# Kernel tuning notes

Measured on AMD Instinct MI355X. Metric: run time of the kernel, lower is better.

The kernel has to match this reference:

```python
import jax, jax.numpy as jnp
import numpy as np

N, IN_DIM, OUT_DIM = 8192, 1024, 256
AVG_DEG = 32


def _w(key, shape, scale=0.05):
    return jax.random.normal(key, shape, dtype=jnp.float32) * scale


def setup_inputs() -> dict:
    key = jax.random.key(0)
    ks = jax.random.split(key, 20)
    x = jax.random.normal(ks[0], (N, IN_DIM), dtype=jnp.float32)
    # binary adjacency with average degree ~AVG_DEG (adj_matrix_to_edge_index
    # only keeps indices, so edge weights are effectively 1)
    A_pos = (jax.random.uniform(ks[1], (N, N)) < (AVG_DEG / N)).astype(jnp.float32)
    d = {"x": x, "A_pos": A_pos}
    # Linear layers (stored as [in, out]; y = x @ W + b)
    d["W1"], d["b1"] = _w(ks[2], (IN_DIM, 256)), jnp.zeros((256,), jnp.float32)
    d["W2"], d["b2"] = _w(ks[3], (256, 62)), jnp.zeros((62,), jnp.float32)
    d["W3"], d["b3"] = _w(ks[4], (62, OUT_DIM)), jnp.zeros((OUT_DIM,), jnp.float32)
    # GCNConv weights/biases
    d["G1"], d["gb1"] = _w(ks[5], (256, 256)), jnp.zeros((256,), jnp.float32)
    d["G2"], d["gb2"] = _w(ks[6], (62, 62)), jnp.zeros((62,), jnp.float32)
    for i, k in zip(range(3, 7), ks[7:11]):
        d[f"G{i}"], d[f"gb{i}"] = _w(k, (OUT_DIM, OUT_DIM)), jnp.zeros((OUT_DIM,), jnp.float32)
    return d


def _gcn_forward(x, A_pos, W1, b1, W2, b2, W3, b3,
                 G1, gb1, G2, gb2, G3, gb3, G4, gb4, G5, gb5, G6, gb6):
    n = x.shape[0]
    # GCN symmetric normalization with self loops: D^{-1/2}(A+I)D^{-1/2}
    A_hat = A_pos + jnp.eye(n, dtype=x.dtype)
    deg = A_hat.sum(axis=1)
    dinv = jnp.where(deg > 0, deg ** -0.5, 0.0)
    A_norm = dinv[:, None] * A_hat * dinv[None, :]

    def gcn(h, W, b):
        return A_norm @ (h @ W) + b

    x1_lin = x @ W1 + b1
    x1 = x1_lin + jax.nn.relu(gcn(x1_lin, G1, gb1))
    x2_lin = x1 @ W2 + b2
    x2 = x2_lin + jax.nn.relu(gcn(x2_lin, G2, gb2))
    x3_lin = x2 @ W3 + b3
    w = 0.5  # self.weight before *= 0.5
    x3 = x3_lin + w * jax.nn.relu(gcn(x3_lin, G3, gb3))
    x4 = x3 + w * jax.nn.relu(gcn(x4_in := x3, G4, gb4))
    w = w * 0.5  # self.weight *= 0.5
    x5 = x4 + w * jax.nn.relu(gcn(x4, G5, gb5))
    x6 = x5 + w * gcn(x5, G6, gb6)
    return x6


def reference(x, A_pos, W1, b1, W2, b2, W3, b3,
              G1, gb1, G2, gb2, G3, gb3, G4, gb4, G5, gb5, G6, gb6):
    return _gcn_forward(x, A_pos, W1, b1, W2, b2, W3, b3,
                        G1, gb1, G2, gb2, G3, gb3, G4, gb4, G5, gb5, G6, gb6)
```

## Files before the change

kernel.cpp:

```cpp
#include <hip/hip_runtime.h>
#include <hip/hip_bf16.h>
#include <stddef.h>
#include <stdint.h>

#define NROWS 8192
#define MAXD 128

typedef __attribute__((ext_vector_type(8))) short bf16x8;
typedef __attribute__((ext_vector_type(4))) float f32x4;
typedef __attribute__((ext_vector_type(4))) unsigned short u16x4;

static __device__ __forceinline__ unsigned short f2bf(float f) {
    unsigned int u = __float_as_uint(f);
    unsigned int r = (u + 0x7FFFu + ((u >> 16) & 1u)) >> 16;
    return (unsigned short)r;
}
static __device__ __forceinline__ float bf2f(unsigned short h) {
    return __uint_as_float(((unsigned int)h) << 16);
}

__global__ __launch_bounds__(256) void build_adj(
    const float* __restrict__ A, int* __restrict__ ell,
    int* __restrict__ cnt, float* __restrict__ dinv)
{
    int row = blockIdx.x;
    const float4* arow = (const float4*)(A + (size_t)row * NROWS);
    __shared__ int scnt;
    if (threadIdx.x == 0) scnt = 0;
    __syncthreads();
    int* erow = ell + (size_t)row * MAXD;
    for (int q = threadIdx.x; q < NROWS / 4; q += 256) {
        float4 v = arow[q];
        int j = q * 4;
        if (v.x != 0.f) { int s = atomicAdd(&scnt, 1); if (s < MAXD) erow[s] = j; }
        if (v.y != 0.f) { int s = atomicAdd(&scnt, 1); if (s < MAXD) erow[s] = j + 1; }
        if (v.z != 0.f) { int s = atomicAdd(&scnt, 1); if (s < MAXD) erow[s] = j + 2; }
        if (v.w != 0.f) { int s = atomicAdd(&scnt, 1); if (s < MAXD) erow[s] = j + 3; }
    }
    __syncthreads();
    if (threadIdx.x == 0) {
        int c = scnt; if (c > MAXD) c = MAXD;
        cnt[row] = c;
        dinv[row] = rsqrtf((float)scnt + 1.0f);
    }
}

__global__ __launch_bounds__(256) void tconv(
    const float* __restrict__ W, unsigned short* __restrict__ ht,
    unsigned short* __restrict__ lt, int K, int N, int Kpad, int Npad)
{
    int idx = blockIdx.x * 256 + threadIdx.x;
    if (idx >= Npad * Kpad) return;
    int n = idx / Kpad, k = idx % Kpad;
    float v = (k < K && n < N) ? W[(size_t)k * N + n] : 0.f;
    unsigned short hv = f2bf(v);
    ht[idx] = hv;
    lt[idx] = f2bf(v - bf2f(hv));
}

__global__ void pad64(const float* __restrict__ src, float* __restrict__ dst, int n)
{
    int i = threadIdx.x;
    dst[i] = (i < n) ? src[i] : 0.f;
}

__global__ __launch_bounds__(256) void gemm_mfma(
    const float* __restrict__ A,
    const unsigned short* __restrict__ Bth, const unsigned short* __restrict__ Btl,
    const float* __restrict__ bias,
    float* __restrict__ C, int K, int N)
{
    __shared__ __attribute__((aligned(16))) char smem[49152];
    const int tid = threadIdx.x;
    const int lane = tid & 63;
    const int w = tid >> 6;
    const int bm0 = blockIdx.x * 128;
    const int bn0 = blockIdx.y * 64;
    const int m_off = (w & 1) * 64;
    const int n_off = (w >> 1) * 32;

    f32x4 acc[4][2];
#pragma unroll
    for (int i = 0; i < 4; i++)
#pragma unroll
        for (int j = 0; j < 2; j++) acc[i][j] = (f32x4){0.f, 0.f, 0.f, 0.f};

    for (int k0 = 0; k0 < K; k0 += 64) {
#pragma unroll
        for (int i = 0; i < 8; ++i) {
            int q = tid + i * 256;
            int row = q >> 4;
            int kq = (q & 15) * 4;
            f32x4 v = *(const f32x4*)(A + (size_t)(bm0 + row) * K + k0 + kq);
            u16x4 hv, lv;
#pragma unroll
            for (int j = 0; j < 4; ++j) {
                unsigned short hh = f2bf(v[j]);
                hv[j] = hh;
                lv[j] = f2bf(v[j] - bf2f(hh));
            }
            int logb = kq * 2;
            int swz = (row << 7) + (logb ^ ((row & 7) << 4));
            *(u16x4*)(smem + swz) = hv;
            *(u16x4*)(smem + 16384 + swz) = lv;
        }
#pragma unroll
        for (int i = 0; i < 4; ++i) {
            int c = tid + i * 256;
            int half = c >> 9;
            int cc = c & 511;
            int row = cc >> 3;
            int logb = (cc & 7) * 16;
            const unsigned short* s =
                (half ? Btl : Bth) + (size_t)(bn0 + row) * K + k0 + (logb >> 1);
            bf16x8 v = *(const bf16x8*)s;
            int swz = (row << 7) + (logb ^ ((row & 7) << 4));
            *(bf16x8*)(smem + 32768 + (half << 13) + swz) = v;
        }
        __syncthreads();

#pragma unroll
        for (int kk = 0; kk < 64; kk += 32) {
            bf16x8 ah[4], al[4], bh[2], bl[2];
            int kb = (kk + ((lane >> 4) * 8)) * 2;
#pragma unroll
            for (int mi = 0; mi < 4; mi++) {
                int row = m_off + mi * 16 + (lane & 15);
                int off = (row << 7) + (kb ^ ((row & 7) << 4));
                ah[mi] = *(const bf16x8*)(smem + off);
                al[mi] = *(const bf16x8*)(smem + 16384 + off);
            }
#pragma unroll
            for (int ni = 0; ni < 2; ni++) {
                int row = n_off + ni * 16 + (lane & 15);
                int off = (row << 7) + (kb ^ ((row & 7) << 4));
                bh[ni] = *(const bf16x8*)(smem + 32768 + off);
                bl[ni] = *(const bf16x8*)(smem + 40960 + off);
            }
#pragma unroll
            for (int mi = 0; mi < 4; mi++)
#pragma unroll
                for (int ni = 0; ni < 2; ni++) {
                    acc[mi][ni] = __builtin_amdgcn_mfma_f32_16x16x32_bf16(ah[mi], bh[ni], acc[mi][ni], 0, 0, 0);
                    acc[mi][ni] = __builtin_amdgcn_mfma_f32_16x16x32_bf16(ah[mi], bl[ni], acc[mi][ni], 0, 0, 0);
                    acc[mi][ni] = __builtin_amdgcn_mfma_f32_16x16x32_bf16(al[mi], bh[ni], acc[mi][ni], 0, 0, 0);
                }
        }
        __syncthreads();
    }

#pragma unroll
    for (int mi = 0; mi < 4; mi++)
#pragma unroll
        for (int ni = 0; ni < 2; ni++) {
            int col = bn0 + n_off + ni * 16 + (lane & 15);
            float bv = bias ? bias[col] : 0.f;
            int rbase = bm0 + m_off + mi * 16 + ((lane >> 4) * 4);
#pragma unroll
            for (int r = 0; r < 4; r++)
                C[(size_t)(rbase + r) * N + col] = acc[mi][ni][r] + bv;
        }
}

__global__ __launch_bounds__(64) void spmm_vec4(
    const float* __restrict__ T, const int* __restrict__ ell,
    const int* __restrict__ cnt, const float* __restrict__ dinv,
    const float* __restrict__ base, const float* __restrict__ gb,
    float* __restrict__ out, float wscale, int do_relu)
{
    __shared__ int nb[MAXD];
    __shared__ float dv[MAXD];
    int row = blockIdx.x;
    int t = threadIdx.x;
    int c = cnt[row];
    for (int e = t; e < c; e += 64) {
        int j = ell[(size_t)row * MAXD + e];
        nb[e] = j;
        dv[e] = dinv[j];
    }
    __syncthreads();
    float di = dinv[row];
    f32x4 r = *(const f32x4*)(T + (size_t)row * 256 + t * 4) * di;
    f32x4 s1 = {0.f,0.f,0.f,0.f}, s2 = {0.f,0.f,0.f,0.f}, s3 = {0.f,0.f,0.f,0.f};
    int e = 0;
    for (; e + 4 <= c; e += 4) {
        r  += dv[e]     * *(const f32x4*)(T + (size_t)nb[e]     * 256 + t * 4);
        s1 += dv[e + 1] * *(const f32x4*)(T + (size_t)nb[e + 1] * 256 + t * 4);
        s2 += dv[e + 2] * *(const f32x4*)(T + (size_t)nb[e + 2] * 256 + t * 4);
        s3 += dv[e + 3] * *(const f32x4*)(T + (size_t)nb[e + 3] * 256 + t * 4);
    }
    for (; e < c; ++e)
        r += dv[e] * *(const f32x4*)(T + (size_t)nb[e] * 256 + t * 4);
    r = (r + s1) + (s2 + s3);
    f32x4 g = *(const f32x4*)(gb + t * 4);
    f32x4 b4 = *(const f32x4*)(base + (size_t)row * 256 + t * 4);
    f32x4 o4;
#pragma unroll
    for (int j = 0; j < 4; ++j) {
        float v = fmaf(di, r[j], g[j]);
        if (do_relu) v = fmaxf(v, 0.f);
        o4[j] = fmaf(wscale, v, b4[j]);
    }
    *(f32x4*)(out + (size_t)row * 256 + t * 4) = o4;
}

__global__ __launch_bounds__(64) void spmm64(
    const float* __restrict__ T, const int* __restrict__ ell,
    const int* __restrict__ cnt, const float* __restrict__ dinv,
    const float* __restrict__ base, const float* __restrict__ gb,
    float* __restrict__ out)
{
    __shared__ int nb[MAXD];
    __shared__ float dv[MAXD];
    int row = blockIdx.x;
    int f = threadIdx.x;
    int c = cnt[row];
    for (int e = f; e < c; e += 64) {
        int j = ell[(size_t)row * MAXD + e];
        nb[e] = j;
        dv[e] = dinv[j];
    }
    __syncthreads();
    float di = dinv[row];
    float r = di * T[(size_t)row * 64 + f];
    float p1 = 0.f, p2 = 0.f, p3 = 0.f;
    int e = 0;
    for (; e + 4 <= c; e += 4) {
        r  = fmaf(dv[e],     T[(size_t)nb[e]     * 64 + f], r);
        p1 = fmaf(dv[e + 1], T[(size_t)nb[e + 1] * 64 + f], p1);
        p2 = fmaf(dv[e + 2], T[(size_t)nb[e + 2] * 64 + f], p2);
        p3 = fmaf(dv[e + 3], T[(size_t)nb[e + 3] * 64 + f], p3);
    }
    for (; e < c; ++e) r = fmaf(dv[e], T[(size_t)nb[e] * 64 + f], r);
    r = (r + p1) + (p2 + p3);
    float v = fmaf(di, r, gb[f]);
    v = fmaxf(v, 0.f);
    out[(size_t)row * 64 + f] = v + base[(size_t)row * 64 + f];
}

static inline void mfma(const float* A, const unsigned short* Bth,
                        const unsigned short* Btl, const float* bias,
                        float* C, int K, int N, hipStream_t s)
{
    dim3 grid(NROWS / 128, N / 64);
    gemm_mfma<<<grid, 256, 0, s>>>(A, Bth, Btl, bias, C, K, N);
}

extern "C" void kernel_launch(void* const* d_in, const int* in_sizes, int n_in,
                              void* d_out, int out_size, void* d_ws, size_t ws_size,
                              hipStream_t stream)
{
    const float* x    = (const float*)d_in[0];
    const float* Apos = (const float*)d_in[1];
    const float* W1 = (const float*)d_in[2];  const float* b1  = (const float*)d_in[3];
    const float* W2 = (const float*)d_in[4];  const float* b2  = (const float*)d_in[5];
    const float* W3 = (const float*)d_in[6];  const float* b3  = (const float*)d_in[7];
    const float* G1 = (const float*)d_in[8];  const float* gb1 = (const float*)d_in[9];
    const float* G2 = (const float*)d_in[10]; const float* gb2 = (const float*)d_in[11];
    const float* G3 = (const float*)d_in[12]; const float* gb3 = (const float*)d_in[13];
    const float* G4 = (const float*)d_in[14]; const float* gb4 = (const float*)d_in[15];
    const float* G5 = (const float*)d_in[16]; const float* gb5 = (const float*)d_in[17];
    const float* G6 = (const float*)d_in[18]; const float* gb6 = (const float*)d_in[19];

    char* ws = (char*)d_ws;
    size_t off = 0;
    auto alloc = [&](size_t bytes) -> void* {
        void* p = ws + off;
        off = (off + bytes + 255) & ~(size_t)255;
        return p;
    };
    int*   ell  = (int*)  alloc((size_t)NROWS * MAXD * 4);
    int*   cnt  = (int*)  alloc((size_t)NROWS * 4);
    float* dinv = (float*)alloc((size_t)NROWS * 4);
    unsigned short* W1th = (unsigned short*)alloc(256 * 1024 * 2);
    unsigned short* W1tl = (unsigned short*)alloc(256 * 1024 * 2);
    unsigned short* W2th = (unsigned short*)alloc(64 * 256 * 2);
    unsigned short* W2tl = (unsigned short*)alloc(64 * 256 * 2);
    unsigned short* W3th = (unsigned short*)alloc(256 * 64 * 2);
    unsigned short* W3tl = (unsigned short*)alloc(256 * 64 * 2);
    unsigned short* G1th = (unsigned short*)alloc(256 * 256 * 2);
    unsigned short* G1tl = (unsigned short*)alloc(256 * 256 * 2);
    unsigned short* G2th = (unsigned short*)alloc(64 * 64 * 2);
    unsigned short* G2tl = (unsigned short*)alloc(64 * 64 * 2);
    unsigned short* G3th = (unsigned short*)alloc(256 * 256 * 2);
    unsigned short* G3tl = (unsigned short*)alloc(256 * 256 * 2);
    unsigned short* G4th = (unsigned short*)alloc(256 * 256 * 2);
    unsigned short* G4tl = (unsigned short*)alloc(256 * 256 * 2);
    unsigned short* G5th = (unsigned short*)alloc(256 * 256 * 2);
    unsigned short* G5tl = (unsigned short*)alloc(256 * 256 * 2);
    unsigned short* G6th = (unsigned short*)alloc(256 * 256 * 2);
    unsigned short* G6tl = (unsigned short*)alloc(256 * 256 * 2);
    float* b2p  = (float*)alloc(64 * 4);
    float* gb2p = (float*)alloc(64 * 4);
    float* lin  = (float*)alloc((size_t)NROWS * 256 * 4);
    float* T    = (float*)alloc((size_t)NROWS * 256 * 4);
    float* hA   = (float*)alloc((size_t)NROWS * 256 * 4);
    float* hB   = (float*)alloc((size_t)NROWS * 256 * 4);
    float* x2lin = lin;
    float* T62   = T;
    float* x2    = hB;
    float* outp = (float*)d_out;

    build_adj<<<NROWS, 256, 0, stream>>>(Apos, ell, cnt, dinv);

    tconv<<<(256 * 1024 + 255) / 256, 256, 0, stream>>>(W1, W1th, W1tl, 1024, 256, 1024, 256);
    tconv<<<(64 * 256 + 255) / 256, 256, 0, stream>>>(W2, W2th, W2tl, 256, 62, 256, 64);
    tconv<<<(256 * 64 + 255) / 256, 256, 0, stream>>>(W3, W3th, W3tl, 62, 256, 64, 256);
    tconv<<<(256 * 256 + 255) / 256, 256, 0, stream>>>(G1, G1th, G1tl, 256, 256, 256, 256);
    tconv<<<(64 * 64 + 255) / 256, 256, 0, stream>>>(G2, G2th, G2tl, 62, 62, 64, 64);
    tconv<<<(256 * 256 + 255) / 256, 256, 0, stream>>>(G3, G3th, G3tl, 256, 256, 256, 256);
    tconv<<<(256 * 256 + 255) / 256, 256, 0, stream>>>(G4, G4th, G4tl, 256, 256, 256, 256);
    tconv<<<(256 * 256 + 255) / 256, 256, 0, stream>>>(G5, G5th, G5tl, 256, 256, 256, 256);
    tconv<<<(256 * 256 + 255) / 256, 256, 0, stream>>>(G6, G6th, G6tl, 256, 256, 256, 256);
    pad64<<<1, 64, 0, stream>>>(b2, b2p, 62);
    pad64<<<1, 64, 0, stream>>>(gb2, gb2p, 62);

    mfma(x, W1th, W1tl, b1, lin, 1024, 256, stream);
    mfma(lin, G1th, G1tl, nullptr, T, 256, 256, stream);
    spmm_vec4<<<NROWS, 64, 0, stream>>>(T, ell, cnt, dinv, lin, gb1, hA, 1.0f, 1);
    mfma(hA, W2th, W2tl, b2p, x2lin, 256, 64, stream);
    mfma(x2lin, G2th, G2tl, nullptr, T62, 64, 64, stream);
    spmm64<<<NROWS, 64, 0, stream>>>(T62, ell, cnt, dinv, x2lin, gb2p, x2);
    mfma(x2, W3th, W3tl, b3, lin, 64, 256, stream);
    mfma(lin, G3th, G3tl, nullptr, T, 256, 256, stream);
    spmm_vec4<<<NROWS, 64, 0, stream>>>(T, ell, cnt, dinv, lin, gb3, hB, 0.5f, 1);
    mfma(hB, G4th, G4tl, nullptr, T, 256, 256, stream);
    spmm_vec4<<<NROWS, 64, 0, stream>>>(T, ell, cnt, dinv, hB, gb4, hA, 0.5f, 1);
    mfma(hA, G5th, G5tl, nullptr, T, 256, 256, stream);
    spmm_vec4<<<NROWS, 64, 0, stream>>>(T, ell, cnt, dinv, hA, gb5, hB, 0.25f, 1);
    mfma(hB, G6th, G6tl, nullptr, T, 256, 256, stream);
    spmm_vec4<<<NROWS, 64, 0, stream>>>(T, ell, cnt, dinv, hB, gb6, outp, 0.25f, 0);
}
```

Before: 812.7 us.

## Store GCN transform outputs as bf16 and gather bf16 in SpMM; batch weight conversions

The GEMM epilogue can now write its output as bf16. The sparse aggregation kernels gather neighbour rows from this bf16 buffer instead of fp32, which halves the bytes moved in the irregular neighbour gathers. The five 256x256 GCN weight conversions and the two bias pads are each merged into a single launch to cut launch count. In exchange, the intermediate h@W values lose precision to bf16 before aggregation, which adds numerical error.

New measurement: 747.3 us. 1.09x faster.

```diff
diff --git a/kernel.cpp b/kernel.cpp
--- a/kernel.cpp
+++ b/kernel.cpp
@@ -17,6 +17,14 @@
 }
 static __device__ __forceinline__ float bf2f(unsigned short h) {
     return __uint_as_float(((unsigned int)h) << 16);
+}
+static __device__ __forceinline__ f32x4 unpack4(uint2 u) {
+    f32x4 f;
+    f[0] = __uint_as_float(u.x << 16);
+    f[1] = __uint_as_float(u.x & 0xFFFF0000u);
+    f[2] = __uint_as_float(u.y << 16);
+    f[3] = __uint_as_float(u.y & 0xFFFF0000u);
+    return f;
 }
 
 __global__ __launch_bounds__(256) void build_adj(
@@ -58,17 +66,45 @@
     lt[idx] = f2bf(v - bf2f(hv));
 }
 
-__global__ void pad64(const float* __restrict__ src, float* __restrict__ dst, int n)
+__global__ __launch_bounds__(256) void tconvG5(
+    const float* __restrict__ g1, const float* __restrict__ g3,
+    const float* __restrict__ g4, const float* __restrict__ g5,
+    const float* __restrict__ g6,
+    unsigned short* __restrict__ h1, unsigned short* __restrict__ l1,
+    unsigned short* __restrict__ h3, unsigned short* __restrict__ l3,
+    unsigned short* __restrict__ h4, unsigned short* __restrict__ l4,
+    unsigned short* __restrict__ h5, unsigned short* __restrict__ l5,
+    unsigned short* __restrict__ h6, unsigned short* __restrict__ l6)
+{
+    const float* s; unsigned short* h; unsigned short* l;
+    switch (blockIdx.y) {
+        case 0:  s = g1; h = h1; l = l1; break;
+        case 1:  s = g3; h = h3; l = l3; break;
+        case 2:  s = g4; h = h4; l = l4; break;
+        case 3:  s = g5; h = h5; l = l5; break;
+        default: s = g6; h = h6; l = l6; break;
+    }
+    int idx = blockIdx.x * 256 + threadIdx.x;
+    int n = idx >> 8, k = idx & 255;
+    float v = s[(size_t)k * 256 + n];
+    unsigned short hv = f2bf(v);
+    h[idx] = hv;
+    l[idx] = f2bf(v - bf2f(hv));
+}
+
+__global__ void pad2(const float* __restrict__ b2, const float* __restrict__ gb2,
+                     float* __restrict__ b2p, float* __restrict__ gb2p)
 {
     int i = threadIdx.x;
-    dst[i] = (i < n) ? src[i] : 0.f;
+    if (i < 64) b2p[i] = (i < 62) ? b2[i] : 0.f;
+    else { int j = i - 64; gb2p[j] = (j < 62) ? gb2[j] : 0.f; }
 }
 
 __global__ __launch_bounds__(256) void gemm_mfma(
     const float* __restrict__ A,
     const unsigned short* __restrict__ Bth, const unsigned short* __restrict__ Btl,
     const float* __restrict__ bias,
-    float* __restrict__ C, int K, int N)
+    float* __restrict__ C, unsigned short* __restrict__ Cb, int K, int N)
 {
     __shared__ __attribute__((aligned(16))) char smem[49152];
     const int tid = threadIdx.x;
@@ -157,13 +193,17 @@
             float bv = bias ? bias[col] : 0.f;
             int rbase = bm0 + m_off + mi * 16 + ((lane >> 4) * 4);
 #pragma unroll
-            for (int r = 0; r < 4; r++)
-                C[(size_t)(rbase + r) * N + col] = acc[mi][ni][r] + bv;
+            for (int r = 0; r < 4; r++) {
+                float v = acc[mi][ni][r] + bv;
+                size_t idx = (size_t)(rbase + r) * N + col;
+                if (C)  C[idx]  = v;
+                if (Cb) Cb[idx] = f2bf(v);
+            }
         }
 }
 
-__global__ __launch_bounds__(64) void spmm_vec4(
-    const float* __restrict__ T, const int* __restrict__ ell,
+__global__ __launch_bounds__(64) void spmm_bf(
+    const unsigned short* __restrict__ Tb, const int* __restrict__ ell,
     const int* __restrict__ cnt, const float* __restrict__ dinv,
     const float* __restrict__ base, const float* __restrict__ gb,
     float* __restrict__ out, float wscale, int do_relu)
@@ -180,17 +220,21 @@
     }
     __syncthreads();
     float di = dinv[row];
-    f32x4 r = *(const f32x4*)(T + (size_t)row * 256 + t * 4) * di;
+    f32x4 r = unpack4(*(const uint2*)(Tb + (size_t)row * 256 + t * 4)) * di;
     f32x4 s1 = {0.f,0.f,0.f,0.f}, s2 = {0.f,0.f,0.f,0.f}, s3 = {0.f,0.f,0.f,0.f};
     int e = 0;
     for (; e + 4 <= c; e += 4) {
-        r  += dv[e]     * *(const f32x4*)(T + (size_t)nb[e]     * 256 + t * 4);
-        s1 += dv[e + 1] * *(const f32x4*)(T + (size_t)nb[e + 1] * 256 + t * 4);
-        s2 += dv[e + 2] * *(const f32x4*)(T + (size_t)nb[e + 2] * 256 + t * 4);
-        s3 += dv[e + 3] * *(const f32x4*)(T + (size_t)nb[e + 3] * 256 + t * 4);
+        uint2 v0 = *(const uint2*)(Tb + (size_t)nb[e]     * 256 + t * 4);
+        uint2 v1 = *(const uint2*)(Tb + (size_t)nb[e + 1] * 256 + t * 4);
+        uint2 v2 = *(const uint2*)(Tb + (size_t)nb[e + 2] * 256 + t * 4);
+        uint2 v3 = *(const uint2*)(Tb + (size_t)nb[e + 3] * 256 + t * 4);
+        r  += dv[e]     * unpack4(v0);
+        s1 += dv[e + 1] * unpack4(v1);
+        s2 += dv[e + 2] * unpack4(v2);
+        s3 += dv[e + 3] * unpack4(v3);
     }
     for (; e < c; ++e)
-        r += dv[e] * *(const f32x4*)(T + (size_t)nb[e] * 256 + t * 4);
+        r += dv[e] * unpack4(*(const uint2*)(Tb + (size_t)nb[e] * 256 + t * 4));
     r = (r + s1) + (s2 + s3);
     f32x4 g = *(const f32x4*)(gb + t * 4);
     f32x4 b4 = *(const f32x4*)(base + (size_t)row * 256 + t * 4);
@@ -204,8 +248,8 @@
     *(f32x4*)(out + (size_t)row * 256 + t * 4) = o4;
 }
 
-__global__ __launch_bounds__(64) void spmm64(
-    const float* __restrict__ T, const int* __restrict__ ell,
+__global__ __launch_bounds__(64) void spmm64_bf(
+    const unsigned short* __restrict__ Tb, const int* __restrict__ ell,
     const int* __restrict__ cnt, const float* __restrict__ dinv,
     const float* __restrict__ base, const float* __restrict__ gb,
     float* __restrict__ out)
@@ -222,16 +266,16 @@
     }
     __syncthreads();
     float di = dinv[row];
-    float r = di * T[(size_t)row * 64 + f];
+    float r = di * bf2f(Tb[(size_t)row * 64 + f]);
     float p1 = 0.f, p2 = 0.f, p3 = 0.f;
     int e = 0;
     for (; e + 4 <= c; e += 4) {
-        r  = fmaf(dv[e],     T[(size_t)nb[e]     * 64 + f], r);
-        p1 = fmaf(dv[e + 1], T[(size_t)nb[e + 1] * 64 + f], p1);
-        p2 = fmaf(dv[e + 2], T[(size_t)nb[e + 2] * 64 + f], p2);
-        p3 = fmaf(dv[e + 3], T[(size_t)nb[e + 3] * 64 + f], p3);
-    }
-    for (; e < c; ++e) r = fmaf(dv[e], T[(size_t)nb[e] * 64 + f], r);
+        r  = fmaf(dv[e],     bf2f(Tb[(size_t)nb[e]     * 64 + f]), r);
+        p1 = fmaf(dv[e + 1], bf2f(Tb[(size_t)nb[e + 1] * 64 + f]), p1);
+        p2 = fmaf(dv[e + 2], bf2f(Tb[(size_t)nb[e + 2] * 64 + f]), p2);
+        p3 = fmaf(dv[e + 3], bf2f(Tb[(size_t)nb[e + 3] * 64 + f]), p3);
+    }
+    for (; e < c; ++e) r = fmaf(dv[e], bf2f(Tb[(size_t)nb[e] * 64 + f]), r);
     r = (r + p1) + (p2 + p3);
     float v = fmaf(di, r, gb[f]);
     v = fmaxf(v, 0.f);
@@ -240,10 +284,10 @@
 
 static inline void mfma(const float* A, const unsigned short* Bth,
                         const unsigned short* Btl, const float* bias,
-                        float* C, int K, int N, hipStream_t s)
+                        float* C, unsigned short* Cb, int K, int N, hipStream_t s)
 {
     dim3 grid(NROWS / 128, N / 64);
-    gemm_mfma<<<grid, 256, 0, s>>>(A, Bth, Btl, bias, C, K, N);
+    gemm_mfma<<<grid, 256, 0, s>>>(A, Bth, Btl, bias, C, Cb, K, N);
 }
 
 extern "C" void kernel_launch(void* const* d_in, const int* in_sizes, int n_in,
@@ -293,11 +337,11 @@
     float* b2p  = (float*)alloc(64 * 4);
     float* gb2p = (float*)alloc(64 * 4);
     float* lin  = (float*)alloc((size_t)NROWS * 256 * 4);
-    float* T    = (float*)alloc((size_t)NROWS * 256 * 4);
+    unsigned short* Tb = (unsigned short*)alloc((size_t)NROWS * 256 * 2);
     float* hA   = (float*)alloc((size_t)NROWS * 256 * 4);
     float* hB   = (float*)alloc((size_t)NROWS * 256 * 4);
     float* x2lin = lin;
-    float* T62   = T;
+    unsigned short* T62b = Tb;
     float* x2    = hB;
     float* outp = (float*)d_out;
 
@@ -306,28 +350,26 @@
     tconv<<<(256 * 1024 + 255) / 256, 256, 0, stream>>>(W1, W1th, W1tl, 1024, 256, 1024, 256);
     tconv<<<(64 * 256 + 255) / 256, 256, 0, stream>>>(W2, W2th, W2tl, 256, 62, 256, 64);
     tconv<<<(256 * 64 + 255) / 256, 256, 0, stream>>>(W3, W3th, W3tl, 62, 256, 64, 256);
-    tconv<<<(256 * 256 + 255) / 256, 256, 0, stream>>>(G1, G1th, G1tl, 256, 256, 256, 256);
     tconv<<<(64 * 64 + 255) / 256, 256, 0, stream>>>(G2, G2th, G2tl, 62, 62, 64, 64);
-    tconv<<<(256 * 256 + 255) / 256, 256, 0, stream>>>(G3, G3th, G3tl, 256, 256, 256, 256);
-    tconv<<<(256 * 256 + 255) / 256, 256, 0, stream>>>(G4, G4th, G4tl, 256, 256, 256, 256);
-    tconv<<<(256 * 256 + 255) / 256, 256, 0, stream>>>(G5, G5th, G5tl, 256, 256, 256, 256);
-    tconv<<<(256 * 256 + 255) / 256, 256, 0, stream>>>(G6, G6th, G6tl, 256, 256, 256, 256);
-    pad64<<<1, 64, 0, stream>>>(b2, b2p, 62);
-    pad64<<<1, 64, 0, stream>>>(gb2, gb2p, 62);
-
-    mfma(x, W1th, W1tl, b1, lin, 1024, 256, stream);
-    mfma(lin, G1th, G1tl, nullptr, T, 256, 256, stream);
-    spmm_vec4<<<NROWS, 64, 0, stream>>>(T, ell, cnt, dinv, lin, gb1, hA, 1.0f, 1);
-    mfma(hA, W2th, W2tl, b2p, x2lin, 256, 64, stream);
-    mfma(x2lin, G2th, G2tl, nullptr, T62, 64, 64, stream);
-    spmm64<<<NROWS, 64, 0, stream>>>(T62, ell, cnt, dinv, x2lin, gb2p, x2);
-    mfma(x2, W3th, W3tl, b3, lin, 64, 256, stream);
-    mfma(lin, G3th, G3tl, nullptr, T, 256, 256, stream);
-    spmm_vec4<<<NROWS, 64, 0, stream>>>(T, ell, cnt, dinv, lin, gb3, hB, 0.5f, 1);
-    mfma(hB, G4th, G4tl, nullptr, T, 256, 256, stream);
-    spmm_vec4<<<NROWS, 64, 0, stream>>>(T, ell, cnt, dinv, hB, gb4, hA, 0.5f, 1);
-    mfma(hA, G5th, G5tl, nullptr, T, 256, 256, stream);
-    spmm_vec4<<<NROWS, 64, 0, stream>>>(T, ell, cnt, dinv, hA, gb5, hB, 0.25f, 1);
-    mfma(hB, G6th, G6tl, nullptr, T, 256, 256, stream);
-    spmm_vec4<<<NROWS, 64, 0, stream>>>(T, ell, cnt, dinv, hB, gb6, outp, 0.25f, 0);
-}
+    dim3 g5(256, 5);
+    tconvG5<<<g5, 256, 0, stream>>>(G1, G3, G4, G5, G6,
+                                    G1th, G1tl, G3th, G3tl, G4th, G4tl,
+                                    G5th, G5tl, G6th, G6tl);
+    pad2<<<1, 128, 0, stream>>>(b2, gb2, b2p, gb2p);
+
+    mfma(x, W1th, W1tl, b1, lin, nullptr, 1024, 256, stream);
+    mfma(lin, G1th, G1tl, nullptr, nullptr, Tb, 256, 256, stream);
+    spmm_bf<<<NROWS, 64, 0, stream>>>(Tb, ell, cnt, dinv, lin, gb1, hA, 1.0f, 1);
+    mfma(hA, W2th, W2tl, b2p, x2lin, nullptr, 256, 64, stream);
+    mfma(x2lin, G2th, G2tl, nullptr, nullptr, T62b, 64, 64, stream);
+    spmm64_bf<<<NROWS, 64, 0, stream>>>(T62b, ell, cnt, dinv, x2lin, gb2p, x2);
+    mfma(x2, W3th, W3tl, b3, lin, nullptr, 64, 256, stream);
+    mfma(lin, G3th, G3tl, nullptr, nullptr, Tb, 256, 256, stream);
+    spmm_bf<<<NROWS, 64, 0, stream>>>(Tb, ell, cnt, dinv, lin, gb3, hB, 0.5f, 1);
+    mfma(hB, G4th, G4tl, nullptr, nullptr, Tb, 256, 256, stream);
+    spmm_bf<<<NROWS, 64, 0, stream>>>(Tb, ell, cnt, dinv, hB, gb4, hA, 0.5f, 1);
+    mfma(hA, G5th, G5tl, nullptr, nullptr, Tb, 256, 256, stream);
+    spmm_bf<<<NROWS, 64, 0, stream>>>(Tb, ell, cnt, dinv, hA, gb5, hB, 0.25f, 1);
+    mfma(hB, G6th, G6tl, nullptr, nullptr, Tb, 256, 256, stream);
+    spmm_bf<<<NROWS, 64, 0, stream>>>(Tb, ell, cnt, dinv, hB, gb6, outp, 0.25f, 0);
+}
```
